# Kernel tuning notes

Hardware: AMD Instinct MI355X
Metric: run time of the kernel (lower is better)

## Reference

```python
import jax, jax.numpy as jnp
import numpy as np

B, L, D = 16, 2048, 128


def setup_inputs() -> dict:
    key = jax.random.key(0)
    k1, k2 = jax.random.split(key)
    x = jax.random.normal(k1, (B, L, D), dtype=jnp.float32)
    mask = jax.random.uniform(k2, (B, L), dtype=jnp.float32)
    return {"input": x, "mask": mask}


def reference(input, mask):
    # mask broadcast over feature dim (torch: mask.unsqueeze(-1).repeat(1,1,D))
    x = input * mask[:, :, None]                       # [B, L, D]
    # attn_weights = bmm(x, x^T) -> [B, L, L]
    scores = jnp.einsum('bld,bmd->blm', x, x)
    # softmax over dim=1 (the FIRST L axis, i.e. columns normalized over rows)
    w = jax.nn.softmax(scores, axis=1)                 # [B, L, L]
    # out = bmm(w^T, x).mean(dim=1, keepdim=True): out_full[b,m,d] = sum_l w[b,l,m] * x[b,l,d]
    out = jnp.einsum('blm,bld->bmd', w, x).mean(axis=1, keepdims=True)  # [B, 1, D]
    attn_mean = w.mean(axis=1)                         # [B, L]
    return (out, attn_mean)
```

## Files before the change

kernel.cpp:

```cpp
#include <hip/hip_runtime.h>
#include <math.h>


constexpr int NB = 16, NL = 2048, ND = 128;
constexpr int ROWS_US = 128;
constexpr int NSLOT = 20;

typedef __attribute__((ext_vector_type(8))) short short8;
typedef __attribute__((ext_vector_type(4))) float f32x4;

#define EXP2(x) __builtin_amdgcn_exp2f(x)

__device__ __forceinline__ unsigned short f2bf(float f) {
  unsigned u = __builtin_bit_cast(unsigned, f);
  u += 0x7FFFu + ((u >> 16) & 1u);
  return (unsigned short)(u >> 16);
}
__device__ __forceinline__ float bf2f(unsigned short h) {
  unsigned u = ((unsigned)h) << 16;
  return __builtin_bit_cast(float, u);
}

__device__ __forceinline__ void stage16(const unsigned short* g, unsigned short* l) {
  __builtin_amdgcn_global_load_lds(
      (const __attribute__((address_space(1))) unsigned int*)g,
      (__attribute__((address_space(3))) unsigned int*)l, 16, 0, 0);
}

__global__ __launch_bounds__(256) void k_prep(const float* __restrict__ x,
                                              const float* __restrict__ mask,
                                              unsigned short* __restrict__ Y,
                                              float* __restrict__ nsq) {
  const int gid = blockIdx.x * 256 + threadIdx.x;
  const int row = gid >> 5;
  const int dq = gid & 31;
  const float4 v = reinterpret_cast<const float4*>(x)[gid];
  const float m = mask[row] * 1.2011224087864498f;
  const unsigned short h0 = f2bf(v.x * m), h1 = f2bf(v.y * m),
                       h2 = f2bf(v.z * m), h3 = f2bf(v.w * m);
  const float g0 = bf2f(h0), g1 = bf2f(h1), g2 = bf2f(h2), g3 = bf2f(h3);
  unsigned short* Yr = Y + (size_t)row * ROWS_US;
  const int sx = dq >> 1, half8 = (dq & 1) * 4;
  const int pos = sx ^ (row & 15);
  *reinterpret_cast<ushort4*>(Yr + pos * 8 + half8) = make_ushort4(h0, h1, h2, h3);
  float ss = g0 * g0 + g1 * g1 + g2 * g2 + g3 * g3;
#pragma unroll
  for (int mk = 1; mk < 32; mk <<= 1) ss += __shfl_xor(ss, mk);
  if (dq == 0) nsq[row] = ss;
}

__global__ __launch_bounds__(256) void k_nmax(const float* __restrict__ nsq,
                                              float* __restrict__ nmax) {
  const int b = blockIdx.x;
  const int tid = threadIdx.x;
  float m = 0.f;
  for (int i = tid; i < NL; i += 256) m = fmaxf(m, nsq[b * NL + i]);
#pragma unroll
  for (int mk = 1; mk < 64; mk <<= 1) m = fmaxf(m, __shfl_xor(m, mk));
  __shared__ float red[4];
  if ((tid & 63) == 0) red[tid >> 6] = m;
  __syncthreads();
  if (tid == 0) nmax[b] = fmaxf(fmaxf(red[0], red[1]), fmaxf(red[2], red[3]));
}

#define STRIP_DECODE()                                     \
  const int sid = blockIdx.x;                              \
  const int idx = sid >> 3;                                \
  const int b = ((sid & 7) << 1) | (idx >> 5);             \
  const int strip = idx & 31;                              \
  const int ib = strip >> 1, hf = strip & 1;               \
  const int d0 = hf * 4;                                   \
  const int nt = (hf == 0) ? 4 : ((ib < 8) ? 5 : 4);       \
  const int row0 = ib * 128;                               \
  const int tid = threadIdx.x;                             \
  const int lane = tid & 63, wave = tid >> 6;              \
  const int wr = wave >> 1, wc = wave & 1;                 \
  const int lhi = lane >> 4, llo = lane & 15;

#define STRIP_A_PROLOGUE(Yb)                                                   \
  _Pragma("unroll") for (int it = 0; it < 8; ++it) {                           \
    const int idx2 = tid + 256 * it;                                           \
    const int r = idx2 >> 4, s = idx2 & 15;                                    \
    stage16(Yb + (size_t)(row0 + r) * ROWS_US + s * 8, At + idx2 * 8);         \
  }                                                                            \
  __syncthreads();                                                             \
  short8 afr[16];                                                              \
  _Pragma("unroll") for (int t4 = 0; t4 < 4; ++t4) {                           \
    const int sl = 4 * t4 + lhi;                                               \
    _Pragma("unroll") for (int qq = 0; qq < 4; ++qq) {                         \
      const int ra = 64 * wr + 16 * qq + llo;                                  \
      afr[t4 * 4 + qq] = *(const short8*)(At + ra * 128 + ((sl ^ (ra & 15)) << 3)); \
    }                                                                          \
  }

#define TILE_GEMM_B(Yb, col0)                                                  \
  f32x4 acc[4][4];                                                             \
  _Pragma("unroll") for (int rs = 0; rs < 4; ++rs)                             \
      _Pragma("unroll") for (int cs = 0; cs < 4; ++cs)                         \
          acc[rs][cs] = f32x4{0.f, 0.f, 0.f, 0.f};                             \
  __syncthreads();                         \
  _Pragma("unroll") for (int it = 0; it < 8; ++it) {                           \
    const int idx2 = tid + 256 * it;                                           \
    const int r = idx2 >> 4, s = idx2 & 15;                                    \
    stage16(Yb + (size_t)(col0 + r) * ROWS_US + s * 8, Bt + idx2 * 8);         \
  }                                                                            \
  __syncthreads();                        \
  _Pragma("unroll") for (int t4 = 0; t4 < 4; ++t4) {                           \
    const int sl = 4 * t4 + lhi;                                               \
    short8 bfx[4];                                                             \
    _Pragma("unroll") for (int qq = 0; qq < 4; ++qq) {                         \
      const int rb = 64 * wc + 16 * qq + llo;                                  \
      bfx[qq] = *(const short8*)(Bt + rb * 128 + ((sl ^ (rb & 15)) << 3));     \
    }                                                                          \
    _Pragma("unroll") for (int rs = 0; rs < 4; ++rs)                           \
        _Pragma("unroll") for (int cs = 0; cs < 4; ++cs)                       \
            acc[rs][cs] = __builtin_amdgcn_mfma_f32_16x16x32_bf16(             \
                afr[t4 * 4 + rs], bfx[cs], acc[rs][cs], 0, 0, 0);              \
  }

__global__ __launch_bounds__(256, 2) void k_esum(const unsigned short* __restrict__ Y,
                                                 const float* __restrict__ nsq,
                                                 const float* __restrict__ nmaxf,
                                                 float* __restrict__ pcs) {
  __shared__ alignas(128) char lds[65536];
  unsigned short* At = (unsigned short*)lds;
  unsigned short* Bt = (unsigned short*)(lds + 32768);
  STRIP_DECODE()
  const unsigned short* Yb = Y + (size_t)b * NL * ROWS_US;
  const float Nmx = nmaxf[b];

  float Cr[16];
#pragma unroll
  for (int rs = 0; rs < 4; ++rs)
#pragma unroll
    for (int rg = 0; rg < 4; ++rg)
      Cr[rs * 4 + rg] = sqrtf(nsq[b * NL + row0 + 64 * wr + 16 * rs + 4 * lhi + rg] * Nmx);

  STRIP_A_PROLOGUE(Yb)

  float racc[16];
#pragma unroll
  for (int i = 0; i < 16; ++i) racc[i] = 0.f;

  for (int dt = 0; dt < nt; ++dt) {
    const int d = d0 + dt;
    const int col0 = ((ib + d) & 15) * 128;
    float Cc[4];
#pragma unroll
    for (int cs = 0; cs < 4; ++cs)
      Cc[cs] = sqrtf(nsq[b * NL + col0 + 64 * wc + 16 * cs + llo] * Nmx);
    TILE_GEMM_B(Yb, col0)
#pragma unroll
    for (int rs = 0; rs < 4; ++rs)
#pragma unroll
      for (int rg = 0; rg < 4; ++rg) {
        float t = 0.f;
#pragma unroll
        for (int cs = 0; cs < 4; ++cs) t += EXP2(acc[rs][cs][rg] - Cr[rs * 4 + rg]);
        racc[rs * 4 + rg] += t;
      }
    if (d != 0) {
      float* dst = pcs + ((size_t)(b * NSLOT + 4 + 2 * (d - 1) + wr)) * NL + col0;
#pragma unroll
      for (int cs = 0; cs < 4; ++cs) {
        float u = 0.f;
#pragma unroll
        for (int rs = 0; rs < 4; ++rs)
#pragma unroll
          for (int rg = 0; rg < 4; ++rg) u += EXP2(acc[rs][cs][rg] - Cc[cs]);
        u += __shfl_xor(u, 16);
        u += __shfl_xor(u, 32);
        if (lhi == 0) dst[64 * wc + 16 * cs + llo] = u;
      }
    }
  }
#pragma unroll
  for (int i = 0; i < 16; ++i) {
    float s = racc[i];
#pragma unroll
    for (int mk = 1; mk < 16; mk <<= 1) s += __shfl_xor(s, mk);
    racc[i] = s;
  }
  if (llo == 0) {
    float* dst = pcs + ((size_t)(b * NSLOT + 2 * hf + wc)) * NL + row0;
#pragma unroll
    for (int rs = 0; rs < 4; ++rs)
#pragma unroll
      for (int rg = 0; rg < 4; ++rg)
        dst[64 * wr + 16 * rs + 4 * lhi + rg] = racc[rs * 4 + rg];
  }
}

__global__ __launch_bounds__(256) void k_comb(const float* __restrict__ pcs,
                                              const float* __restrict__ nsq,
                                              const float* __restrict__ nmaxf,
                                              float* __restrict__ Q) {
  const int i = blockIdx.x * 256 + threadIdx.x;
  const int b = i >> 11, row = i & (NL - 1);
  const int o = row >> 7;
  float s = 0.f;
#pragma unroll
  for (int c = 0; c < NSLOT; ++c) {
    if (c >= 18 && o < 8) continue;
    s += pcs[((size_t)(b * NSLOT + c)) * NL + row];
  }
  Q[i] = -sqrtf(nsq[i] * nmaxf[b]) - __log2f(s);
}

__global__ __launch_bounds__(256, 2) void k_r(const unsigned short* __restrict__ Y,
                                              const float* __restrict__ Qa,
                                              float* __restrict__ rp) {
  __shared__ alignas(128) char lds[65536];
  unsigned short* At = (unsigned short*)lds;
  unsigned short* Bt = (unsigned short*)(lds + 32768);
  STRIP_DECODE()
  const unsigned short* Yb = Y + (size_t)b * NL * ROWS_US;

  float Qr[16];
#pragma unroll
  for (int rs = 0; rs < 4; ++rs)
#pragma unroll
    for (int rg = 0; rg < 4; ++rg)
      Qr[rs * 4 + rg] = Qa[b * NL + row0 + 64 * wr + 16 * rs + 4 * lhi + rg];

  STRIP_A_PROLOGUE(Yb)

  float racc[16];
#pragma unroll
  for (int i = 0; i < 16; ++i) racc[i] = 0.f;

  for (int dt = 0; dt < nt; ++dt) {
    const int d = d0 + dt;
    const int col0 = ((ib + d) & 15) * 128;
    float Qc[4];
#pragma unroll
    for (int cs = 0; cs < 4; ++cs) Qc[cs] = Qa[b * NL + col0 + 64 * wc + 16 * cs + llo];
    TILE_GEMM_B(Yb, col0)
#pragma unroll
    for (int rs = 0; rs < 4; ++rs)
#pragma unroll
      for (int rg = 0; rg < 4; ++rg) {
        float t = 0.f;
#pragma unroll
        for (int cs = 0; cs < 4; ++cs) t += EXP2(acc[rs][cs][rg] + Qc[cs]);
        racc[rs * 4 + rg] += t;
      }
    if (d != 0) {
      float* dst = rp + ((size_t)(b * NSLOT + 4 + 2 * (d - 1) + wr)) * NL + col0;
#pragma unroll
      for (int cs = 0; cs < 4; ++cs) {
        float u = 0.f;
#pragma unroll
        for (int rs = 0; rs < 4; ++rs)
#pragma unroll
          for (int rg = 0; rg < 4; ++rg) u += EXP2(acc[rs][cs][rg] + Qr[rs * 4 + rg]);
        u += __shfl_xor(u, 16);
        u += __shfl_xor(u, 32);
        if (lhi == 0) dst[64 * wc + 16 * cs + llo] = u;
      }
    }
  }
#pragma unroll
  for (int i = 0; i < 16; ++i) {
    float s = racc[i];
#pragma unroll
    for (int mk = 1; mk < 16; mk <<= 1) s += __shfl_xor(s, mk);
    racc[i] = s;
  }
  if (llo == 0) {
    float* dst = rp + ((size_t)(b * NSLOT + 2 * hf + wc)) * NL + row0;
#pragma unroll
    for (int rs = 0; rs < 4; ++rs)
#pragma unroll
      for (int rg = 0; rg < 4; ++rg)
        dst[64 * wr + 16 * rs + 4 * lhi + rg] = racc[rs * 4 + rg];
  }
}

__global__ __launch_bounds__(256) void k_outp(const float* __restrict__ x,
                                              const float* __restrict__ mask,
                                              const float* __restrict__ rp,
                                              float* __restrict__ partial) {
  const int b = blockIdx.y;
  const int seg = blockIdx.x;
  const int tid = threadIdx.x;
  const int l0 = seg * 128;
  __shared__ float w_s[128];
  __shared__ float4 red[8][32];
  if (tid < 128) {
    float s = 0.f;
#pragma unroll
    for (int c = 0; c < NSLOT; ++c) {
      if (c >= 18 && seg < 8) continue;
      s += rp[((size_t)(b * NSLOT + c)) * NL + l0 + tid];
    }
    w_s[tid] = s * mask[b * NL + l0 + tid];
  }
  __syncthreads();
  const int dq = tid & 31;
  const int rg = tid >> 5;
  float4 acc = make_float4(0.f, 0.f, 0.f, 0.f);
#pragma unroll 4
  for (int i = 0; i < 16; ++i) {
    const int l = 8 * i + rg;
    const float w = w_s[l];
    const float4 v = *reinterpret_cast<const float4*>(x + ((size_t)b * NL + l0 + l) * ND + 4 * dq);
    acc.x += w * v.x; acc.y += w * v.y; acc.z += w * v.z; acc.w += w * v.w;
  }
  red[rg][dq] = acc;
  __syncthreads();
  if (rg == 0) {
    float4 s = acc;
#pragma unroll
    for (int k = 1; k < 8; ++k) {
      const float4 t = red[k][dq];
      s.x += t.x; s.y += t.y; s.z += t.z; s.w += t.w;
    }
    *reinterpret_cast<float4*>(partial + ((size_t)(b * 16 + seg)) * ND + 4 * dq) = s;
  }
}

__global__ __launch_bounds__(1024) void k_fin(const float* __restrict__ partial,
                                              float* __restrict__ out) {
  const int gid = blockIdx.x * 1024 + threadIdx.x;
  if (gid < NB * ND) {
    const int b = gid >> 7, d = gid & (ND - 1);
    float s = 0.f;
#pragma unroll
    for (int k = 0; k < 16; ++k) s += partial[(size_t)(b * 16 + k) * ND + d];
    out[gid] = s * (1.0f / NL);
  }
  out[NB * ND + gid] = 1.0f / NL;
}

extern "C" void kernel_launch(void* const* d_in, const int* in_sizes, int n_in,
                              void* d_out, int out_size, void* d_ws, size_t ws_size,
                              hipStream_t stream) {
  const float* x = (const float*)d_in[0];
  const float* mask = (const float*)d_in[1];
  float* out = (float*)d_out;

  unsigned short* Y = (unsigned short*)d_ws;
  float* nsq = (float*)(Y + (size_t)NB * NL * ROWS_US);
  float* nmaxf = nsq + NB * NL;
  float* pcs = nmaxf + 16;
  float* rp = pcs;
  float* Q = pcs + (size_t)NB * NSLOT * NL;
  float* partial = Q + NB * NL;

  k_prep<<<dim3(NB * NL * ND / 4 / 256), 256, 0, stream>>>(x, mask, Y, nsq);
  k_nmax<<<NB, 256, 0, stream>>>(nsq, nmaxf);
  k_esum<<<dim3(512), 256, 0, stream>>>(Y, nsq, nmaxf, pcs);
  k_comb<<<dim3(NB * NL / 256), 256, 0, stream>>>(pcs, nsq, nmaxf, Q);
  k_r<<<dim3(512), 256, 0, stream>>>(Y, Q, rp);
  k_outp<<<dim3(16, NB), 256, 0, stream>>>(x, mask, rp, partial);
  k_fin<<<32, 1024, 0, stream>>>(partial, out);
}
```

Before: 67.93 us.

## Double-buffer B tiles in LDS to overlap global staging with MFMA

In both strip GEMM kernels (k_esum and k_r), the next column tile is now staged into a second LDS buffer while MFMAs and the exp epilogue run on the current tile. The buffer that held the A strip is reused as the second B buffer once the A fragments have been hoisted into registers. The per-tile wait on global-to-LDS loads before compute is replaced by a single barrier at the end of each iteration. This hides load latency behind compute without adding LDS, but it depends on the barrier draining the async loads before the buffer is read.

```diff
diff --git a/kernel.cpp b/kernel.cpp
--- a/kernel.cpp
+++ b/kernel.cpp
@@ -77,45 +77,39 @@
   const int wr = wave >> 1, wc = wave & 1;                 \
   const int lhi = lane >> 4, llo = lane & 15;
 
-#define STRIP_A_PROLOGUE(Yb)                                                   \
-  _Pragma("unroll") for (int it = 0; it < 8; ++it) {                           \
-    const int idx2 = tid + 256 * it;                                           \
-    const int r = idx2 >> 4, s = idx2 & 15;                                    \
-    stage16(Yb + (size_t)(row0 + r) * ROWS_US + s * 8, At + idx2 * 8);         \
-  }                                                                            \
-  __syncthreads();                                                             \
-  short8 afr[16];                                                              \
-  _Pragma("unroll") for (int t4 = 0; t4 < 4; ++t4) {                           \
-    const int sl = 4 * t4 + lhi;                                               \
-    _Pragma("unroll") for (int qq = 0; qq < 4; ++qq) {                         \
-      const int ra = 64 * wr + 16 * qq + llo;                                  \
-      afr[t4 * 4 + qq] = *(const short8*)(At + ra * 128 + ((sl ^ (ra & 15)) << 3)); \
-    }                                                                          \
-  }
-
-#define TILE_GEMM_B(Yb, col0)                                                  \
-  f32x4 acc[4][4];                                                             \
-  _Pragma("unroll") for (int rs = 0; rs < 4; ++rs)                             \
-      _Pragma("unroll") for (int cs = 0; cs < 4; ++cs)                         \
-          acc[rs][cs] = f32x4{0.f, 0.f, 0.f, 0.f};                             \
-  __syncthreads();                         \
-  _Pragma("unroll") for (int it = 0; it < 8; ++it) {                           \
-    const int idx2 = tid + 256 * it;                                           \
-    const int r = idx2 >> 4, s = idx2 & 15;                                    \
-    stage16(Yb + (size_t)(col0 + r) * ROWS_US + s * 8, Bt + idx2 * 8);         \
-  }                                                                            \
-  __syncthreads();                        \
-  _Pragma("unroll") for (int t4 = 0; t4 < 4; ++t4) {                           \
-    const int sl = 4 * t4 + lhi;                                               \
-    short8 bfx[4];                                                             \
-    _Pragma("unroll") for (int qq = 0; qq < 4; ++qq) {                         \
-      const int rb = 64 * wc + 16 * qq + llo;                                  \
-      bfx[qq] = *(const short8*)(Bt + rb * 128 + ((sl ^ (rb & 15)) << 3));     \
-    }                                                                          \
-    _Pragma("unroll") for (int rs = 0; rs < 4; ++rs)                           \
-        _Pragma("unroll") for (int cs = 0; cs < 4; ++cs)                       \
-            acc[rs][cs] = __builtin_amdgcn_mfma_f32_16x16x32_bf16(             \
-                afr[t4 * 4 + rs], bfx[cs], acc[rs][cs], 0, 0, 0);              \
+#define STAGE_TILE(dst, Yb, r0)                                            \
+  _Pragma("unroll") for (int it = 0; it < 8; ++it) {                       \
+    const int idx2 = tid + 256 * it;                                       \
+    const int r = idx2 >> 4, s = idx2 & 15;                                \
+    stage16((Yb) + (size_t)((r0) + r) * ROWS_US + s * 8, (dst) + idx2 * 8); \
+  }
+
+#define HOIST_A(src)                                                        \
+  short8 afr[16];                                                           \
+  _Pragma("unroll") for (int t4 = 0; t4 < 4; ++t4) {                        \
+    const int sl = 4 * t4 + lhi;                                            \
+    _Pragma("unroll") for (int qq = 0; qq < 4; ++qq) {                      \
+      const int ra = 64 * wr + 16 * qq + llo;                               \
+      afr[t4 * 4 + qq] = *(const short8*)((src) + ra * 128 + ((sl ^ (ra & 15)) << 3)); \
+    }                                                                       \
+  }
+
+#define TILE_MFMA(src)                                                      \
+  f32x4 acc[4][4];                                                          \
+  _Pragma("unroll") for (int rs = 0; rs < 4; ++rs)                          \
+      _Pragma("unroll") for (int cs = 0; cs < 4; ++cs)                      \
+          acc[rs][cs] = f32x4{0.f, 0.f, 0.f, 0.f};                          \
+  _Pragma("unroll") for (int t4 = 0; t4 < 4; ++t4) {                        \
+    const int sl = 4 * t4 + lhi;                                            \
+    short8 bfx[4];                                                          \
+    _Pragma("unroll") for (int qq = 0; qq < 4; ++qq) {                      \
+      const int rb = 64 * wc + 16 * qq + llo;                               \
+      bfx[qq] = *(const short8*)((src) + rb * 128 + ((sl ^ (rb & 15)) << 3)); \
+    }                                                                       \
+    _Pragma("unroll") for (int rs = 0; rs < 4; ++rs)                        \
+        _Pragma("unroll") for (int cs = 0; cs < 4; ++cs)                    \
+            acc[rs][cs] = __builtin_amdgcn_mfma_f32_16x16x32_bf16(          \
+                afr[t4 * 4 + rs], bfx[cs], acc[rs][cs], 0, 0, 0);           \
   }
 
 __global__ __launch_bounds__(256, 2) void k_esum(const unsigned short* __restrict__ Y,
@@ -123,8 +117,8 @@
                                                  const float* __restrict__ nmaxf,
                                                  float* __restrict__ pcs) {
   __shared__ alignas(128) char lds[65536];
-  unsigned short* At = (unsigned short*)lds;
-  unsigned short* Bt = (unsigned short*)(lds + 32768);
+  unsigned short* B1 = (unsigned short*)lds;
+  unsigned short* B0 = (unsigned short*)(lds + 32768);
   STRIP_DECODE()
   const unsigned short* Yb = Y + (size_t)b * NL * ROWS_US;
   const float Nmx = nmaxf[b];
@@ -136,7 +130,11 @@
     for (int rg = 0; rg < 4; ++rg)
       Cr[rs * 4 + rg] = sqrtf(nsq[b * NL + row0 + 64 * wr + 16 * rs + 4 * lhi + rg] * Nmx);
 
-  STRIP_A_PROLOGUE(Yb)
+  STAGE_TILE(B1, Yb, row0)
+  STAGE_TILE(B0, Yb, ((ib + d0) & 15) * 128)
+  __syncthreads();
+  HOIST_A(B1)
+  __syncthreads();
 
   float racc[16];
 #pragma unroll
@@ -145,11 +143,16 @@
   for (int dt = 0; dt < nt; ++dt) {
     const int d = d0 + dt;
     const int col0 = ((ib + d) & 15) * 128;
+    unsigned short* cur = (dt & 1) ? B1 : B0;
+    if (dt + 1 < nt) {
+      unsigned short* nxt = (dt & 1) ? B0 : B1;
+      STAGE_TILE(nxt, Yb, ((ib + d + 1) & 15) * 128)
+    }
     float Cc[4];
 #pragma unroll
     for (int cs = 0; cs < 4; ++cs)
       Cc[cs] = sqrtf(nsq[b * NL + col0 + 64 * wc + 16 * cs + llo] * Nmx);
-    TILE_GEMM_B(Yb, col0)
+    TILE_MFMA(cur)
 #pragma unroll
     for (int rs = 0; rs < 4; ++rs)
 #pragma unroll
@@ -173,6 +176,7 @@
         if (lhi == 0) dst[64 * wc + 16 * cs + llo] = u;
       }
     }
+    __syncthreads();
   }
 #pragma unroll
   for (int i = 0; i < 16; ++i) {
@@ -211,8 +215,8 @@
                                               const float* __restrict__ Qa,
                                               float* __restrict__ rp) {
   __shared__ alignas(128) char lds[65536];
-  unsigned short* At = (unsigned short*)lds;
-  unsigned short* Bt = (unsigned short*)(lds + 32768);
+  unsigned short* B1 = (unsigned short*)lds;
+  unsigned short* B0 = (unsigned short*)(lds + 32768);
   STRIP_DECODE()
   const unsigned short* Yb = Y + (size_t)b * NL * ROWS_US;
 
@@ -223,7 +227,11 @@
     for (int rg = 0; rg < 4; ++rg)
       Qr[rs * 4 + rg] = Qa[b * NL + row0 + 64 * wr + 16 * rs + 4 * lhi + rg];
 
-  STRIP_A_PROLOGUE(Yb)
+  STAGE_TILE(B1, Yb, row0)
+  STAGE_TILE(B0, Yb, ((ib + d0) & 15) * 128)
+  __syncthreads();
+  HOIST_A(B1)
+  __syncthreads();
 
   float racc[16];
 #pragma unroll
@@ -232,10 +240,15 @@
   for (int dt = 0; dt < nt; ++dt) {
     const int d = d0 + dt;
     const int col0 = ((ib + d) & 15) * 128;
+    unsigned short* cur = (dt & 1) ? B1 : B0;
+    if (dt + 1 < nt) {
+      unsigned short* nxt = (dt & 1) ? B0 : B1;
+      STAGE_TILE(nxt, Yb, ((ib + d + 1) & 15) * 128)
+    }
     float Qc[4];
 #pragma unroll
     for (int cs = 0; cs < 4; ++cs) Qc[cs] = Qa[b * NL + col0 + 64 * wc + 16 * cs + llo];
-    TILE_GEMM_B(Yb, col0)
+    TILE_MFMA(cur)
 #pragma unroll
     for (int rs = 0; rs < 4; ++rs)
 #pragma unroll
@@ -259,6 +272,7 @@
         if (lhi == 0) dst[64 * wc + 16 * cs + llo] = u;
       }
     }
+    __syncthreads();
   }
 #pragma unroll
   for (int i = 0; i < 16; ++i) {
```

New measurement: 67.95 us. About the same (+0.0%).

## Split column tiles into halves, drop A register cache, raise occupancy to 3

Applied to the files above, without the earlier changes.

Each 128-column B tile is now staged and processed as two 64-column halves, which shrinks the LDS footprint from 64KB to 48KB per block. The A fragments are no longer held in registers for the whole strip and are re-read from LDS every iteration, and launch bounds go from 2 to 3 blocks per CU. The aim is more resident waves to hide the memory and exp latency. The cost is extra LDS reads, twice as many barriers, and tighter register limits that could cause spills.

```diff
diff --git a/kernel.cpp b/kernel.cpp
--- a/kernel.cpp
+++ b/kernel.cpp
@@ -77,52 +77,47 @@
   const int wr = wave >> 1, wc = wave & 1;                 \
   const int lhi = lane >> 4, llo = lane & 15;
 
-#define STRIP_A_PROLOGUE(Yb)                                                   \
-  _Pragma("unroll") for (int it = 0; it < 8; ++it) {                           \
-    const int idx2 = tid + 256 * it;                                           \
-    const int r = idx2 >> 4, s = idx2 & 15;                                    \
-    stage16(Yb + (size_t)(row0 + r) * ROWS_US + s * 8, At + idx2 * 8);         \
-  }                                                                            \
-  __syncthreads();                                                             \
-  short8 afr[16];                                                              \
-  _Pragma("unroll") for (int t4 = 0; t4 < 4; ++t4) {                           \
-    const int sl = 4 * t4 + lhi;                                               \
-    _Pragma("unroll") for (int qq = 0; qq < 4; ++qq) {                         \
-      const int ra = 64 * wr + 16 * qq + llo;                                  \
-      afr[t4 * 4 + qq] = *(const short8*)(At + ra * 128 + ((sl ^ (ra & 15)) << 3)); \
-    }                                                                          \
-  }
-
-#define TILE_GEMM_B(Yb, col0)                                                  \
-  f32x4 acc[4][4];                                                             \
-  _Pragma("unroll") for (int rs = 0; rs < 4; ++rs)                             \
-      _Pragma("unroll") for (int cs = 0; cs < 4; ++cs)                         \
-          acc[rs][cs] = f32x4{0.f, 0.f, 0.f, 0.f};                             \
-  __syncthreads();                         \
-  _Pragma("unroll") for (int it = 0; it < 8; ++it) {                           \
-    const int idx2 = tid + 256 * it;                                           \
-    const int r = idx2 >> 4, s = idx2 & 15;                                    \
-    stage16(Yb + (size_t)(col0 + r) * ROWS_US + s * 8, Bt + idx2 * 8);         \
-  }                                                                            \
-  __syncthreads();                        \
-  _Pragma("unroll") for (int t4 = 0; t4 < 4; ++t4) {                           \
-    const int sl = 4 * t4 + lhi;                                               \
-    short8 bfx[4];                                                             \
-    _Pragma("unroll") for (int qq = 0; qq < 4; ++qq) {                         \
-      const int rb = 64 * wc + 16 * qq + llo;                                  \
-      bfx[qq] = *(const short8*)(Bt + rb * 128 + ((sl ^ (rb & 15)) << 3));     \
-    }                                                                          \
-    _Pragma("unroll") for (int rs = 0; rs < 4; ++rs)                           \
-        _Pragma("unroll") for (int cs = 0; cs < 4; ++cs)                       \
-            acc[rs][cs] = __builtin_amdgcn_mfma_f32_16x16x32_bf16(             \
-                afr[t4 * 4 + rs], bfx[cs], acc[rs][cs], 0, 0, 0);              \
-  }
-
-__global__ __launch_bounds__(256, 2) void k_esum(const unsigned short* __restrict__ Y,
+#define STAGE_AT(dst, Yb, r0)                                               \
+  _Pragma("unroll") for (int it = 0; it < 8; ++it) {                        \
+    const int idx2 = tid + 256 * it;                                        \
+    const int r = idx2 >> 4, s = idx2 & 15;                                 \
+    stage16((Yb) + (size_t)((r0) + r) * ROWS_US + s * 8, (dst) + idx2 * 8); \
+  }
+
+#define STAGE_BH(dst, Yb, c0)                                               \
+  _Pragma("unroll") for (int it = 0; it < 4; ++it) {                        \
+    const int idx2 = tid + 256 * it;                                        \
+    const int r = idx2 >> 4, s = idx2 & 15;                                 \
+    stage16((Yb) + (size_t)((c0) + r) * ROWS_US + s * 8, (dst) + idx2 * 8); \
+  }
+
+#define HALF_MFMA(Atp, Btp)                                                  \
+  f32x4 acc[4][2];                                                           \
+  _Pragma("unroll") for (int rs = 0; rs < 4; ++rs)                           \
+      _Pragma("unroll") for (int cs = 0; cs < 2; ++cs)                       \
+          acc[rs][cs] = f32x4{0.f, 0.f, 0.f, 0.f};                           \
+  _Pragma("unroll") for (int t4 = 0; t4 < 4; ++t4) {                         \
+    const int sl = 4 * t4 + lhi;                                             \
+    short8 af[4], bf[2];                                                     \
+    _Pragma("unroll") for (int qq = 0; qq < 4; ++qq) {                       \
+      const int ra = 64 * wr + 16 * qq + llo;                                \
+      af[qq] = *(const short8*)((Atp) + ra * 128 + ((sl ^ (ra & 15)) << 3)); \
+    }                                                                        \
+    _Pragma("unroll") for (int cs = 0; cs < 2; ++cs) {                       \
+      const int rb = 32 * wc + 16 * cs + llo;                                \
+      bf[cs] = *(const short8*)((Btp) + rb * 128 + ((sl ^ (rb & 15)) << 3)); \
+    }                                                                        \
+    _Pragma("unroll") for (int rs = 0; rs < 4; ++rs)                         \
+        _Pragma("unroll") for (int cs = 0; cs < 2; ++cs)                     \
+            acc[rs][cs] = __builtin_amdgcn_mfma_f32_16x16x32_bf16(           \
+                af[rs], bf[cs], acc[rs][cs], 0, 0, 0);                       \
+  }
+
+__global__ __launch_bounds__(256, 3) void k_esum(const unsigned short* __restrict__ Y,
                                                  const float* __restrict__ nsq,
                                                  const float* __restrict__ nmaxf,
                                                  float* __restrict__ pcs) {
-  __shared__ alignas(128) char lds[65536];
+  __shared__ alignas(128) char lds[49152];
   unsigned short* At = (unsigned short*)lds;
   unsigned short* Bt = (unsigned short*)(lds + 32768);
   STRIP_DECODE()
@@ -136,7 +131,7 @@
     for (int rg = 0; rg < 4; ++rg)
       Cr[rs * 4 + rg] = sqrtf(nsq[b * NL + row0 + 64 * wr + 16 * rs + 4 * lhi + rg] * Nmx);
 
-  STRIP_A_PROLOGUE(Yb)
+  STAGE_AT(At, Yb, row0)
 
   float racc[16];
 #pragma unroll
@@ -145,32 +140,36 @@
   for (int dt = 0; dt < nt; ++dt) {
     const int d = d0 + dt;
     const int col0 = ((ib + d) & 15) * 128;
-    float Cc[4];
-#pragma unroll
-    for (int cs = 0; cs < 4; ++cs)
-      Cc[cs] = sqrtf(nsq[b * NL + col0 + 64 * wc + 16 * cs + llo] * Nmx);
-    TILE_GEMM_B(Yb, col0)
-#pragma unroll
-    for (int rs = 0; rs < 4; ++rs)
-#pragma unroll
-      for (int rg = 0; rg < 4; ++rg) {
-        float t = 0.f;
-#pragma unroll
-        for (int cs = 0; cs < 4; ++cs) t += EXP2(acc[rs][cs][rg] - Cr[rs * 4 + rg]);
-        racc[rs * 4 + rg] += t;
-      }
-    if (d != 0) {
-      float* dst = pcs + ((size_t)(b * NSLOT + 4 + 2 * (d - 1) + wr)) * NL + col0;
-#pragma unroll
-      for (int cs = 0; cs < 4; ++cs) {
-        float u = 0.f;
-#pragma unroll
-        for (int rs = 0; rs < 4; ++rs)
-#pragma unroll
-          for (int rg = 0; rg < 4; ++rg) u += EXP2(acc[rs][cs][rg] - Cc[cs]);
-        u += __shfl_xor(u, 16);
-        u += __shfl_xor(u, 32);
-        if (lhi == 0) dst[64 * wc + 16 * cs + llo] = u;
+#pragma unroll
+    for (int h = 0; h < 2; ++h) {
+      const int colh = col0 + 64 * h;
+      __syncthreads();
+      STAGE_BH(Bt, Yb, colh)
+      float Cc[2];
+#pragma unroll
+      for (int cs = 0; cs < 2; ++cs)
+        Cc[cs] = sqrtf(nsq[b * NL + colh + 32 * wc + 16 * cs + llo] * Nmx);
+      __syncthreads();
+      HALF_MFMA(At, Bt)
+#pragma unroll
+      for (int rs = 0; rs < 4; ++rs)
+#pragma unroll
+        for (int rg = 0; rg < 4; ++rg)
+          racc[rs * 4 + rg] += EXP2(acc[rs][0][rg] - Cr[rs * 4 + rg]) +
+                               EXP2(acc[rs][1][rg] - Cr[rs * 4 + rg]);
+      if (d != 0) {
+        float* dst = pcs + ((size_t)(b * NSLOT + 4 + 2 * (d - 1) + wr)) * NL + colh;
+#pragma unroll
+        for (int cs = 0; cs < 2; ++cs) {
+          float u = 0.f;
+#pragma unroll
+          for (int rs = 0; rs < 4; ++rs)
+#pragma unroll
+            for (int rg = 0; rg < 4; ++rg) u += EXP2(acc[rs][cs][rg] - Cc[cs]);
+          u += __shfl_xor(u, 16);
+          u += __shfl_xor(u, 32);
+          if (lhi == 0) dst[32 * wc + 16 * cs + llo] = u;
+        }
       }
     }
   }
@@ -207,10 +206,10 @@
   Q[i] = -sqrtf(nsq[i] * nmaxf[b]) - __log2f(s);
 }
 
-__global__ __launch_bounds__(256, 2) void k_r(const unsigned short* __restrict__ Y,
+__global__ __launch_bounds__(256, 3) void k_r(const unsigned short* __restrict__ Y,
                                               const float* __restrict__ Qa,
                                               float* __restrict__ rp) {
-  __shared__ alignas(128) char lds[65536];
+  __shared__ alignas(128) char lds[49152];
   unsigned short* At = (unsigned short*)lds;
   unsigned short* Bt = (unsigned short*)(lds + 32768);
   STRIP_DECODE()
@@ -223,7 +222,7 @@
     for (int rg = 0; rg < 4; ++rg)
       Qr[rs * 4 + rg] = Qa[b * NL + row0 + 64 * wr + 16 * rs + 4 * lhi + rg];
 
-  STRIP_A_PROLOGUE(Yb)
+  STAGE_AT(At, Yb, row0)
 
   float racc[16];
 #pragma unroll
@@ -232,31 +231,36 @@
   for (int dt = 0; dt < nt; ++dt) {
     const int d = d0 + dt;
     const int col0 = ((ib + d) & 15) * 128;
-    float Qc[4];
-#pragma unroll
-    for (int cs = 0; cs < 4; ++cs) Qc[cs] = Qa[b * NL + col0 + 64 * wc + 16 * cs + llo];
-    TILE_GEMM_B(Yb, col0)
-#pragma unroll
-    for (int rs = 0; rs < 4; ++rs)
-#pragma unroll
-      for (int rg = 0; rg < 4; ++rg) {
-        float t = 0.f;
-#pragma unroll
-        for (int cs = 0; cs < 4; ++cs) t += EXP2(acc[rs][cs][rg] + Qc[cs]);
-        racc[rs * 4 + rg] += t;
-      }
-    if (d != 0) {
-      float* dst = rp + ((size_t)(b * NSLOT + 4 + 2 * (d - 1) + wr)) * NL + col0;
-#pragma unroll
-      for (int cs = 0; cs < 4; ++cs) {
-        float u = 0.f;
-#pragma unroll
-        for (int rs = 0; rs < 4; ++rs)
-#pragma unroll
-          for (int rg = 0; rg < 4; ++rg) u += EXP2(acc[rs][cs][rg] + Qr[rs * 4 + rg]);
-        u += __shfl_xor(u, 16);
-        u += __shfl_xor(u, 32);
-        if (lhi == 0) dst[64 * wc + 16 * cs + llo] = u;
+#pragma unroll
+    for (int h = 0; h < 2; ++h) {
+      const int colh = col0 + 64 * h;
+      __syncthreads();
+      STAGE_BH(Bt, Yb, colh)
+      float Qc[2];
+#pragma unroll
+      for (int cs = 0; cs < 2; ++cs)
+        Qc[cs] = Qa[b * NL + colh + 32 * wc + 16 * cs + llo];
+      __syncthreads();
+      HALF_MFMA(At, Bt)
+#pragma unroll
+      for (int rs = 0; rs < 4; ++rs)
+#pragma unroll
+        for (int rg = 0; rg < 4; ++rg)
+          racc[rs * 4 + rg] += EXP2(acc[rs][0][rg] + Qc[0]) +
+                               EXP2(acc[rs][1][rg] + Qc[1]);
+      if (d != 0) {
+        float* dst = rp + ((size_t)(b * NSLOT + 4 + 2 * (d - 1) + wr)) * NL + colh;
+#pragma unroll
+        for (int cs = 0; cs < 2; ++cs) {
+          float u = 0.f;
+#pragma unroll
+          for (int rs = 0; rs < 4; ++rs)
+#pragma unroll
+            for (int rg = 0; rg < 4; ++rg) u += EXP2(acc[rs][cs][rg] + Qr[rs * 4 + rg]);
+          u += __shfl_xor(u, 16);
+          u += __shfl_xor(u, 32);
+          if (lhi == 0) dst[32 * wc + 16 * cs + llo] = u;
+        }
       }
     }
   }
```

Result: slower. 69.59 us (+2.4%).
